# Kernel optimization log

Hardware: AMD Instinct MI355X
Metric: run time of the kernel (lower is better)

## Reference

```python
import jax, jax.numpy as jnp
import numpy as np

B, N, IN_DIM, HID, OUT, E = 2, 50000, 64, 256, 128, 500000

def setup_inputs() -> dict:
    key = jax.random.key(0)
    ks = jax.random.split(key, 8)
    s = lambda fan_in: 1.0 / np.sqrt(fan_in)
    x = jax.random.normal(ks[0], (B, N, IN_DIM), dtype=jnp.float32)
    edges = jax.random.randint(ks[1], (E, 2), 0, N, dtype=jnp.int64)
    return {
        "x": x,
        "edges": edges,
        "ew1": jax.random.normal(ks[2], (2 * IN_DIM, HID), dtype=jnp.float32) * s(2 * IN_DIM),
        "eb1": jnp.zeros((HID,), jnp.float32),
        "ew2": jax.random.normal(ks[3], (HID, OUT), dtype=jnp.float32) * s(HID),
        "eb2": jnp.zeros((OUT,), jnp.float32),
        "nw1": jax.random.normal(ks[4], (IN_DIM, HID), dtype=jnp.float32) * s(IN_DIM),
        "nb1": jnp.zeros((HID,), jnp.float32),
        "nw2": jax.random.normal(ks[5], (HID, OUT), dtype=jnp.float32) * s(HID),
        "nb2": jnp.zeros((OUT,), jnp.float32),
        "dw": jax.random.normal(ks[6], (OUT, IN_DIM), dtype=jnp.float32) * s(OUT),
        "db": jnp.zeros((IN_DIM,), jnp.float32),
    }

def _mlp(z, w1, b1, w2, b2):
    return jax.nn.relu(z @ w1 + b1) @ w2 + b2

def reference(x, edges, ew1, eb1, ew2, eb2, nw1, nb1, nw2, nb2, dw, db):
    u, v = edges[:, 0], edges[:, 1]
    # node embedding: [B, N, OUT]
    h = _mlp(x, nw1, nb1, nw2, nb2)
    # per-edge MLP on concatenated endpoint features: [B, E, OUT]
    edge_input = jnp.concatenate([x[:, u], x[:, v]], axis=-1)  # [B, E, 2*IN]
    edge_emb = _mlp(edge_input, ew1, eb1, ew2, eb2)
    # scatter-add edge message to both endpoints
    messages = jnp.zeros_like(h).at[:, u].add(edge_emb).at[:, v].add(edge_emb)
    h = h + messages
    recon = h @ dw + db  # [B, N, IN]
    return recon
```

## Files before the change

### kernel.cpp

```cpp
#include <hip/hip_runtime.h>
#include <hip/hip_bf16.h>

#define BB   2
#define NN   50000
#define BN   100000
#define NE   500000
#define NSB  196

using u16 = unsigned short;
using u32 = unsigned int;
typedef __attribute__((ext_vector_type(8))) short short8;
typedef __attribute__((ext_vector_type(8))) _Float16 half8;
typedef __attribute__((ext_vector_type(4))) float f32x4;

__device__ __forceinline__ u16 f2bf(float f) {
    union { float f; u32 u; } w; w.f = f;
    return (u16)((w.u + 0x7fffu + ((w.u >> 16) & 1u)) >> 16);
}
__device__ __forceinline__ u16 f2h(float f) {
    _Float16 h = (_Float16)f; u16 u; __builtin_memcpy(&u, &h, 2); return u;
}

#if defined(__has_builtin)
#if __has_builtin(__builtin_amdgcn_cvt_pk_bf16_f32)
#define HAVE_CVTPK 1
#endif
#if __has_builtin(__builtin_amdgcn_cvt_pkrtz)
#define HAVE_PKRTZ 1
#endif
#endif

__device__ __forceinline__ u32 pack_bf(float lo, float hi) {
#ifdef HAVE_CVTPK
    auto r = __builtin_amdgcn_cvt_pk_bf16_f32(lo, hi);
    u32 out; __builtin_memcpy(&out, &r, sizeof(out));
    return out;
#else
    return ((u32)f2bf(hi) << 16) | (u32)f2bf(lo);
#endif
}

__device__ __forceinline__ u32 pack_h2(float lo, float hi) {
#ifdef HAVE_PKRTZ
    auto r = __builtin_amdgcn_cvt_pkrtz(lo, hi);
    u32 out; __builtin_memcpy(&out, &r, sizeof(out));
    return out;
#else
    return ((u32)f2h(hi) << 16) | (u32)f2h(lo);
#endif
}

__device__ __forceinline__ u32 pk_add_h2(u32 a, u32 b) {
    u32 d; asm("v_pk_add_f16 %0, %1, %2" : "=v"(d) : "v"(a), "v"(b)); return d;
}
__device__ __forceinline__ u32 pk_relu_h2(u32 a) {
    u32 d, z = 0u;
    asm("v_pk_max_f16 %0, %1, %2" : "=v"(d) : "v"(a), "v"(z)); return d;
}
__device__ __forceinline__ half8 as_h8(short8 s) {
    half8 h; __builtin_memcpy(&h, &s, 16); return h;
}

__global__ __launch_bounds__(256) void csr_zero2(int* __restrict__ a, int* __restrict__ b) {
    int i = blockIdx.x * 256 + threadIdx.x;
    if (i < NN) { a[i] = 0; b[i] = 0; }
}

__global__ __launch_bounds__(256) void csr_hist2(const int* __restrict__ edges,
                                                 int* __restrict__ curU,
                                                 int* __restrict__ curV) {
    int e = blockIdx.x * 256 + threadIdx.x;
    if (e < NE) {
        atomicAdd(&curU[edges[2*e]], 1);
        atomicAdd(&curV[edges[2*e+1]], 1);
    }
}

__global__ __launch_bounds__(256) void scan_pass1(const int* __restrict__ cursor,
                                                  int* __restrict__ bsum) {
    __shared__ int s[256];
    const int t = threadIdx.x;
    int i = blockIdx.x * 256 + t;
    s[t] = (i < NN) ? cursor[i] : 0;
    __syncthreads();
    for (int d = 128; d > 0; d >>= 1) {
        if (t < d) s[t] += s[t + d];
        __syncthreads();
    }
    if (t == 0) bsum[blockIdx.x] = s[0];
}

__global__ __launch_bounds__(256) void scan_pass2(const int* __restrict__ bsum,
                                                  int* __restrict__ boff) {
    __shared__ int s[256];
    const int t = threadIdx.x;
    s[t] = (t < NSB) ? bsum[t] : 0;
    __syncthreads();
    for (int d = 1; d < 256; d <<= 1) {
        int v = (t >= d) ? s[t - d] : 0;
        __syncthreads();
        s[t] += v;
        __syncthreads();
    }
    if (t <= NSB) boff[t] = (t == 0) ? 0 : s[t - 1];
}

__global__ __launch_bounds__(256) void scan_pass3(int* __restrict__ cursor,
                                                  const int* __restrict__ boff,
                                                  int* __restrict__ off) {
    __shared__ int s[256];
    const int t = threadIdx.x;
    int i = blockIdx.x * 256 + t;
    int v = (i < NN) ? cursor[i] : 0;
    s[t] = v;
    __syncthreads();
    for (int d = 1; d < 256; d <<= 1) {
        int p = (t >= d) ? s[t - d] : 0;
        __syncthreads();
        s[t] += p;
        __syncthreads();
    }
    int excl = boff[blockIdx.x] + s[t] - v;
    if (i < NN) { off[i] = excl; cursor[i] = excl; }
    if (i == NN - 1) off[NN] = excl + v;
}

__global__ __launch_bounds__(256) void csr_fillU(const int* __restrict__ edges,
                                                 int* __restrict__ curU,
                                                 int* __restrict__ ueidx,
                                                 int* __restrict__ upos) {
    int e = blockIdx.x * 256 + threadIdx.x;
    if (e < NE) {
        int s = atomicAdd(&curU[edges[2*e]], 1);
        ueidx[s] = e;
        upos[e] = s;
    }
}

__global__ __launch_bounds__(256) void csr_fillV(const int* __restrict__ edges,
                                                 int* __restrict__ curV,
                                                 const int* __restrict__ upos,
                                                 int* __restrict__ vmap) {
    int e = blockIdx.x * 256 + threadIdx.x;
    if (e < NE) {
        int s = atomicAdd(&curV[edges[2*e+1]], 1);
        vmap[s] = upos[e];
    }
}

__global__ __launch_bounds__(256) void weight_prep(
    const float* __restrict__ ew1, const float* __restrict__ nw1,
    const float* __restrict__ ew2, const float* __restrict__ nw2,
    const float* __restrict__ dw,  const float* __restrict__ db,
    const float* __restrict__ eb2, const float* __restrict__ nb2,
    u16* __restrict__ frag, float* __restrict__ bias2)
{
    int blk = blockIdx.x, t = threadIdx.x;
    if (blk < 192) {
        int idx = blk * 256 + t;
        const float* src; int KB, local;
        if (idx < 32768) { local = idx;         src = ew1; KB = 4; }
        else             { local = idx - 32768; src = nw1; KB = 2; }
        int j = local & 7, l = (local >> 3) & 63, rest = local >> 9;
        int kblk = rest % KB, ntile = rest / KB;
        int n = ntile * 16 + (l & 15);
        int k = kblk * 32 + ((l >> 4) << 3) + j;
        frag[idx] = f2bf(src[k * 256 + n]);
    } else if (blk < 320) {
        int idx = (blk - 192) * 256 + t;
        bool is_e = (idx < 16384);
        const float* src = is_e ? ew2 : nw2;
        int local = idx & 16383;
        int j = local & 7, l = (local >> 3) & 63, rest = local >> 9;
        int kblk = rest & 7, ntile = rest >> 3;
        int n = ntile * 16 + (l & 15);
        int k = kblk * 32 + ((l >> 4) << 3) + j;
        float s = 0.f;
        for (int jj = 0; jj < 128; ++jj) s = fmaf(src[k * 128 + jj], dw[jj * 64 + n], s);
        frag[49152 + idx] = is_e ? f2h(s) : f2bf(s);
    } else if (t < 128) {
        int d = t & 63;
        const float* bsrc = (t >= 64) ? nb2 : eb2;
        float s = 0.f;
        #pragma unroll 4
        for (int j = 0; j < 128; ++j) s = fmaf(bsrc[j], dw[j * 64 + d], s);
        if (t >= 64) bias2[64 + d] = s + db[d];
        else         bias2[d] = s;
    }
}

__global__ __launch_bounds__(256) void node_mlp_kernel(
    const float* __restrict__ x, const float* __restrict__ nb1,
    const float* __restrict__ bias2, const u16* __restrict__ frag,
    u16* __restrict__ xbf, float* __restrict__ out)
{
    __shared__ u16 xs[64 * 64];
    __shared__ u16 hid[64 * 256];
    const int t = threadIdx.x;
    const int wave = t >> 6, l = t & 63, lane15 = l & 15, quad = l >> 4;
    const int r0 = blockIdx.x * 64;
    const int valid = min(64, BN - r0);

    #pragma unroll
    for (int it = 0; it < 4; ++it) {
        int i = t + it * 256;
        int m = i >> 4, c4 = i & 15;
        int row = min(r0 + m, BN - 1);
        float4 g = ((const float4*)x)[(size_t)row * 16 + c4];
        uint2 q = make_uint2(pack_bf(g.x, g.y), pack_bf(g.z, g.w));
        int chunk = c4 >> 1;
        *(uint2*)(xs + m * 64 + ((chunk ^ (m & 7)) << 3) + (c4 & 1) * 4) = q;
        *(uint2*)(xbf + (size_t)row * 64 + c4 * 4) = q;
    }
    __syncthreads();

    {
        f32x4 acc[4][4];
        #pragma unroll
        for (int i = 0; i < 4; ++i)
            #pragma unroll
            for (int mt = 0; mt < 4; ++mt) acc[i][mt] = f32x4{0.f,0.f,0.f,0.f};
        const u16* w1 = frag + 32768;
        #pragma unroll
        for (int kblk = 0; kblk < 2; ++kblk) {
            short8 bf[4], af[4];
            int chunk = kblk * 4 + quad;
            #pragma unroll
            for (int mt = 0; mt < 4; ++mt) {
                int row = mt*16 + lane15;
                bf[mt] = *(const short8*)(xs + row * 64 + ((chunk ^ (row & 7)) << 3));
            }
            #pragma unroll
            for (int i = 0; i < 4; ++i)
                af[i] = *(const short8*)(w1 + (((wave*4 + i)*2 + kblk)*64 + l) * 8);
            #pragma unroll
            for (int i = 0; i < 4; ++i)
                #pragma unroll
                for (int mt = 0; mt < 4; ++mt)
                    acc[i][mt] = __builtin_amdgcn_mfma_f32_16x16x32_bf16(af[i], bf[mt], acc[i][mt], 0, 0, 0);
        }
        #pragma unroll
        for (int i = 0; i < 4; ++i) {
            int n0 = (wave*4 + i)*16 + quad*4;
            int chunk = (wave*4 + i)*2 + (quad >> 1);
            float4 bv = *(const float4*)(nb1 + n0);
            #pragma unroll
            for (int mt = 0; mt < 4; ++mt) {
                int row = mt*16 + lane15;
                uint2 q = make_uint2(
                    pack_bf(fmaxf(acc[i][mt][0] + bv.x, 0.f), fmaxf(acc[i][mt][1] + bv.y, 0.f)),
                    pack_bf(fmaxf(acc[i][mt][2] + bv.z, 0.f), fmaxf(acc[i][mt][3] + bv.w, 0.f)));
                *(uint2*)(hid + row * 256 + ((chunk ^ (row & 15)) << 3) + (quad & 1) * 4) = q;
            }
        }
    }
    __syncthreads();

    {
        f32x4 acc[4];
        #pragma unroll
        for (int mt = 0; mt < 4; ++mt) acc[mt] = f32x4{0.f,0.f,0.f,0.f};
        const u16* w2 = frag + 65536;
        #pragma unroll
        for (int kblk = 0; kblk < 8; ++kblk) {
            short8 bf[4], af;
            int chunk = kblk * 4 + quad;
            #pragma unroll
            for (int mt = 0; mt < 4; ++mt) {
                int row = mt*16 + lane15;
                bf[mt] = *(const short8*)(hid + row * 256 + ((chunk ^ (row & 15)) << 3));
            }
            af = *(const short8*)(w2 + ((wave*8 + kblk)*64 + l) * 8);
            #pragma unroll
            for (int mt = 0; mt < 4; ++mt)
                acc[mt] = __builtin_amdgcn_mfma_f32_16x16x32_bf16(af, bf[mt], acc[mt], 0, 0, 0);
        }
        int n0 = wave*16 + quad*4;
        float4 bv = *(const float4*)(bias2 + 64 + n0);
        #pragma unroll
        for (int mt = 0; mt < 4; ++mt) {
            int m = mt*16 + lane15;
            if (m < valid) {
                float4 o;
                o.x = acc[mt][0] + bv.x; o.y = acc[mt][1] + bv.y;
                o.z = acc[mt][2] + bv.z; o.w = acc[mt][3] + bv.w;
                *(float4*)(out + (size_t)(r0 + m) * 64 + n0) = o;
            }
        }
    }
}

__global__ __launch_bounds__(256) void edge_pre_kernel(
    const u16* __restrict__ xbf, const float* __restrict__ eb1,
    const u16* __restrict__ frag, u16* __restrict__ At, u16* __restrict__ Ab,
    int b)
{
    __shared__ u16 xs[64 * 64];
    __shared__ u16 stg[64 * 256];
    const int t = threadIdx.x;
    const int wave = t >> 6, l = t & 63, lane15 = l & 15, quad = l >> 4;
    const int r0 = blockIdx.x * 64;
    const int valid = min(64, NN - r0);

    #pragma unroll
    for (int it = 0; it < 2; ++it) {
        int i = t + it * 256;
        int m = i >> 3, c = i & 7;
        int row = min(r0 + m, NN - 1);
        uint4 q = ((const uint4*)xbf)[((size_t)(b * NN + row)) * 8 + c];
        *(uint4*)(xs + m * 64 + ((c ^ (m & 7)) << 3)) = q;
    }
    __syncthreads();

    const u16* w1 = frag;
    for (int T = 0; T < 2; ++T) {
        f32x4 acc[4][4];
        #pragma unroll
        for (int i = 0; i < 4; ++i)
            #pragma unroll
            for (int mt = 0; mt < 4; ++mt) acc[i][mt] = f32x4{0.f,0.f,0.f,0.f};
        #pragma unroll
        for (int kblk = 0; kblk < 2; ++kblk) {
            short8 bf[4], af[4];
            int chunk = kblk * 4 + quad;
            #pragma unroll
            for (int mt = 0; mt < 4; ++mt) {
                int row = mt*16 + lane15;
                bf[mt] = *(const short8*)(xs + row * 64 + ((chunk ^ (row & 7)) << 3));
            }
            #pragma unroll
            for (int i = 0; i < 4; ++i)
                af[i] = *(const short8*)(w1 + (((wave*4 + i)*4 + T*2 + kblk)*64 + l) * 8);
            #pragma unroll
            for (int i = 0; i < 4; ++i)
                #pragma unroll
                for (int mt = 0; mt < 4; ++mt)
                    acc[i][mt] = __builtin_amdgcn_mfma_f32_16x16x32_bf16(af[i], bf[mt], acc[i][mt], 0, 0, 0);
        }
        #pragma unroll
        for (int i = 0; i < 4; ++i) {
            int ntile = wave*4 + i;
            int n0 = ntile*16 + quad*4;
            float4 bv;
            if (T == 0) bv = *(const float4*)(eb1 + n0);
            else        bv = make_float4(0.f, 0.f, 0.f, 0.f);
            int c16 = ntile*2 + (quad >> 1);
            #pragma unroll
            for (int mt = 0; mt < 4; ++mt) {
                int row = mt*16 + lane15;
                uint2 q = make_uint2(
                    pack_h2(acc[i][mt][0] + bv.x, acc[i][mt][1] + bv.y),
                    pack_h2(acc[i][mt][2] + bv.z, acc[i][mt][3] + bv.w));
                *(uint2*)(stg + row * 256 + ((c16 ^ (row & 7)) << 3) + (quad & 1) * 4) = q;
            }
        }
        __syncthreads();
        u16* dst = (T == 0) ? At : Ab;
        #pragma unroll
        for (int it = 0; it < 8; ++it) {
            int i = t + it * 256;
            int m = i >> 5, c = i & 31;
            if (m < valid)
                ((uint4*)dst)[((size_t)(r0 + m)) * 32 + c] =
                    *(const uint4*)(stg + m * 256 + ((c ^ (m & 7)) << 3));
        }
        __syncthreads();
    }
}

__global__ __launch_bounds__(256) void edge_emb2_kernel(
    const u16* __restrict__ At, const u16* __restrict__ Ab,
    const int* __restrict__ edges, const int* __restrict__ ueidx,
    const float* __restrict__ bias2,
    const u16* __restrict__ frag, u16* __restrict__ perm)
{
    __shared__ u16 hid[64 * 128];
    __shared__ int us[64], vs[64];
    const int t = threadIdx.x;
    const int wave = t >> 6, l = t & 63, lane15 = l & 15, quad = l >> 4;
    const int e0 = blockIdx.x * 64;
    const int valid = min(64, NE - e0);

    if (t < 64) {
        int j = min(e0 + t, NE - 1);
        int e = ueidx[j];
        us[t] = edges[2 * e];
        vs[t] = edges[2 * e + 1];
    }
    __syncthreads();

    f32x4 acc[4];
    #pragma unroll
    for (int mt = 0; mt < 4; ++mt) acc[mt] = f32x4{0.f,0.f,0.f,0.f};
    const u16* w2 = frag + 49152;

    #pragma unroll
    for (int half = 0; half < 2; ++half) {
        #pragma unroll
        for (int it = 0; it < 4; ++it) {
            int i = t + it * 256;
            int m = i >> 4, c = i & 15;
            int cg = half * 16 + c;
            int u = us[m], v = vs[m];
            uint4 a = ((const uint4*)At)[(size_t)((u32)u) * 32 + cg];
            uint4 bq = ((const uint4*)Ab)[(size_t)((u32)v) * 32 + cg];
            uint4 r;
            r.x = pk_relu_h2(pk_add_h2(a.x, bq.x));
            r.y = pk_relu_h2(pk_add_h2(a.y, bq.y));
            r.z = pk_relu_h2(pk_add_h2(a.z, bq.z));
            r.w = pk_relu_h2(pk_add_h2(a.w, bq.w));
            *(uint4*)(hid + m * 128 + ((c ^ (m & 15)) << 3)) = r;
        }
        __syncthreads();

        #pragma unroll
        for (int kb = 0; kb < 4; ++kb) {
            short8 bf[4], af;
            int chunk = kb * 4 + quad;
            #pragma unroll
            for (int mt = 0; mt < 4; ++mt) {
                int row = mt*16 + lane15;
                bf[mt] = *(const short8*)(hid + row * 128 + ((chunk ^ (row & 15)) << 3));
            }
            af = *(const short8*)(w2 + ((wave*8 + half*4 + kb)*64 + l) * 8);
            #pragma unroll
            for (int mt = 0; mt < 4; ++mt)
                acc[mt] = __builtin_amdgcn_mfma_f32_16x16x32_f16(as_h8(af), as_h8(bf[mt]), acc[mt], 0, 0, 0);
        }
        __syncthreads();
    }

    {
        int n0 = wave*16 + quad*4;
        int chunk = wave*2 + (quad >> 1);
        float4 bv = *(const float4*)(bias2 + n0);
        #pragma unroll
        for (int mt = 0; mt < 4; ++mt) {
            int m = mt*16 + lane15;
            uint2 q = make_uint2(
                pack_bf(acc[mt][0] + bv.x, acc[mt][1] + bv.y),
                pack_bf(acc[mt][2] + bv.z, acc[mt][3] + bv.w));
            *(uint2*)(hid + m * 64 + ((chunk ^ (m & 7)) << 3) + (quad & 1) * 4) = q;
        }
    }
    __syncthreads();

    #pragma unroll
    for (int it = 0; it < 2; ++it) {
        int i = t + it * 256;
        int m = i >> 3, c8 = i & 7;
        if (m < valid)
            ((uint4*)perm)[((size_t)(e0 + m)) * 8 + c8] =
                *(const uint4*)(hid + m * 64 + ((c8 ^ (m & 7)) << 3));
    }
}

__global__ __launch_bounds__(256) void gather3_kernel(
    const u32* __restrict__ perm32, const int* __restrict__ uoff,
    const int* __restrict__ voff, const int* __restrict__ vmap,
    float* __restrict__ out, int b)
{
    const int t = threadIdx.x, wave = t >> 6, l = t & 63;
    const int n = blockIdx.x * 4 + wave;
    const int ub = uoff[n], ucnt = uoff[n + 1] - ub;
    const int vb = voff[n], vcnt = voff[n + 1] - vb;
    if ((ucnt | vcnt) == 0) return;
    const int slot = l >> 4, c8h = l & 15;
    float a0 = 0.f, a1 = 0.f, a2 = 0.f, a3 = 0.f;

    for (int j0 = 0; j0 < ucnt; j0 += 8) {
        int jA = j0 + slot, jB = j0 + 4 + slot;
        const u32* rpA = perm32 + (size_t)(ub + min(jA, ucnt - 1)) * 32 + 2 * c8h;
        const u32* rpB = perm32 + (size_t)(ub + min(jB, ucnt - 1)) * 32 + 2 * c8h;
        u32 wA0 = rpA[0], wA1 = rpA[1];
        u32 wB0 = rpB[0], wB1 = rpB[1];
        union { u32 u; float f; } x0, x1, x2, x3;
        if (jA < ucnt) {
            x0.u = wA0 << 16; x1.u = wA0 & 0xffff0000u;
            x2.u = wA1 << 16; x3.u = wA1 & 0xffff0000u;
            a0 += x0.f; a1 += x1.f; a2 += x2.f; a3 += x3.f;
        }
        if (jB < ucnt) {
            x0.u = wB0 << 16; x1.u = wB0 & 0xffff0000u;
            x2.u = wB1 << 16; x3.u = wB1 & 0xffff0000u;
            a0 += x0.f; a1 += x1.f; a2 += x2.f; a3 += x3.f;
        }
    }
    for (int j0 = 0; j0 < vcnt; j0 += 8) {
        int jA = j0 + slot, jB = j0 + 4 + slot;
        int pA = vmap[vb + min(jA, vcnt - 1)];
        int pB = vmap[vb + min(jB, vcnt - 1)];
        const u32* rpA = perm32 + (size_t)pA * 32 + 2 * c8h;
        const u32* rpB = perm32 + (size_t)pB * 32 + 2 * c8h;
        u32 wA0 = rpA[0], wA1 = rpA[1];
        u32 wB0 = rpB[0], wB1 = rpB[1];
        union { u32 u; float f; } x0, x1, x2, x3;
        if (jA < vcnt) {
            x0.u = wA0 << 16; x1.u = wA0 & 0xffff0000u;
            x2.u = wA1 << 16; x3.u = wA1 & 0xffff0000u;
            a0 += x0.f; a1 += x1.f; a2 += x2.f; a3 += x3.f;
        }
        if (jB < vcnt) {
            x0.u = wB0 << 16; x1.u = wB0 & 0xffff0000u;
            x2.u = wB1 << 16; x3.u = wB1 & 0xffff0000u;
            a0 += x0.f; a1 += x1.f; a2 += x2.f; a3 += x3.f;
        }
    }

    a0 += __shfl_xor(a0, 16); a1 += __shfl_xor(a1, 16);
    a2 += __shfl_xor(a2, 16); a3 += __shfl_xor(a3, 16);
    a0 += __shfl_xor(a0, 32); a1 += __shfl_xor(a1, 32);
    a2 += __shfl_xor(a2, 32); a3 += __shfl_xor(a3, 32);
    if (l < 16) {
        float4* p = (float4*)(out + (size_t)(b * NN + n) * 64 + 4 * l);
        float4 h = *p;
        h.x += a0; h.y += a1; h.z += a2; h.w += a3;
        *p = h;
    }
}

extern "C" void kernel_launch(void* const* d_in, const int* in_sizes, int n_in,
                              void* d_out, int out_size, void* d_ws, size_t ws_size,
                              hipStream_t stream) {
    const float* x     = (const float*)d_in[0];
    const int*   edges = (const int*)d_in[1];
    const float* ew1   = (const float*)d_in[2];
    const float* eb1   = (const float*)d_in[3];
    const float* ew2   = (const float*)d_in[4];
    const float* eb2   = (const float*)d_in[5];
    const float* nw1   = (const float*)d_in[6];
    const float* nb1   = (const float*)d_in[7];
    const float* nw2   = (const float*)d_in[8];
    const float* nb2   = (const float*)d_in[9];
    const float* dw    = (const float*)d_in[10];
    const float* db    = (const float*)d_in[11];
    float* out = (float*)d_out;

    char* w = (char*)d_ws;
    size_t o = 0;
    auto take = [&](size_t bytes) { char* p = w + o; o = (o + bytes + 511) & ~(size_t)511; return p; };
    u16*   frag   = (u16*)  take(81920 * 2);
    float* bias2  = (float*)take(128 * 4);
    int*   curU   = (int*)  take((size_t)NN * 4);
    int*   curV   = (int*)  take((size_t)NN * 4);
    int*   uoff   = (int*)  take((size_t)(NN + 1) * 4);
    int*   voff   = (int*)  take((size_t)(NN + 1) * 4);
    int*   bsum   = (int*)  take((size_t)(NSB + 1) * 4);
    int*   boff   = (int*)  take((size_t)(NSB + 1) * 4);
    int*   ueidx  = (int*)  take((size_t)NE * 4);
    int*   upos   = (int*)  take((size_t)NE * 4);
    int*   vmap   = (int*)  take((size_t)NE * 4);
    u16*   xbf    = (u16*)  take((size_t)BN * 64 * 2);
    u16*   At     = (u16*)  take((size_t)NN * 256 * 2);
    u16*   Ab     = (u16*)  take((size_t)NN * 256 * 2);
    u16*   perm   = (u16*)  take((size_t)NE * 64 * 2);

    csr_zero2<<<NSB, 256, 0, stream>>>(curU, curV);
    csr_hist2<<<(NE + 255) / 256, 256, 0, stream>>>(edges, curU, curV);
    scan_pass1<<<NSB, 256, 0, stream>>>(curU, bsum);
    scan_pass2<<<1, 256, 0, stream>>>(bsum, boff);
    scan_pass3<<<NSB, 256, 0, stream>>>(curU, boff, uoff);
    scan_pass1<<<NSB, 256, 0, stream>>>(curV, bsum);
    scan_pass2<<<1, 256, 0, stream>>>(bsum, boff);
    scan_pass3<<<NSB, 256, 0, stream>>>(curV, boff, voff);
    csr_fillU<<<(NE + 255) / 256, 256, 0, stream>>>(edges, curU, ueidx, upos);
    csr_fillV<<<(NE + 255) / 256, 256, 0, stream>>>(edges, curV, upos, vmap);

    weight_prep<<<321, 256, 0, stream>>>(ew1, nw1, ew2, nw2, dw, db, eb2, nb2, frag, bias2);

    node_mlp_kernel<<<(BN + 63) / 64, 256, 0, stream>>>(x, nb1, bias2, frag, xbf, out);

    for (int b = 0; b < BB; ++b) {
        edge_pre_kernel<<<(NN + 63) / 64, 256, 0, stream>>>(xbf, eb1, frag, At, Ab, b);
        edge_emb2_kernel<<<(NE + 63) / 64, 256, 0, stream>>>(At, Ab, edges, ueidx, bias2, frag, perm);
        gather3_kernel<<<NN / 4, 256, 0, stream>>>((const u32*)perm, uoff, voff, vmap, out, b);
    }
}
```

Measured before the change: 457.5 us.

## Fuse CSR build, node MLP and edge precompute; process both batches per edge launch

Folds the edge-degree histogram into the weight-prep launch and the first scan pass into the node MLP launch. The node MLP kernel now also computes the per-node edge first-layer projections (At/Ab) for both batches, which removes the separate xbf buffer and the edge_pre kernel. The edge embedding and gather kernels handle both batches in one launch, storing u/v pairs in CSR order and gathering 128-wide rows. This cuts the number of launches and lets the per-edge and per-node index work be shared across batches, at the cost of larger intermediate buffers and more work per block.

New measurement: 407.3 us. 1.12x faster.

```diff
diff --git a/kernel.cpp b/kernel.cpp
--- a/kernel.cpp
+++ b/kernel.cpp
@@ -6,6 +6,7 @@
 #define BN   100000
 #define NE   500000
 #define NSB  196
+#define NODE_NB 1563
 
 using u16 = unsigned short;
 using u32 = unsigned int;
@@ -61,101 +62,23 @@
     half8 h; __builtin_memcpy(&h, &s, 16); return h;
 }
 
-__global__ __launch_bounds__(256) void csr_zero2(int* __restrict__ a, int* __restrict__ b) {
-    int i = blockIdx.x * 256 + threadIdx.x;
-    if (i < NN) { a[i] = 0; b[i] = 0; }
-}
-
-__global__ __launch_bounds__(256) void csr_hist2(const int* __restrict__ edges,
-                                                 int* __restrict__ curU,
-                                                 int* __restrict__ curV) {
-    int e = blockIdx.x * 256 + threadIdx.x;
-    if (e < NE) {
-        atomicAdd(&curU[edges[2*e]], 1);
-        atomicAdd(&curV[edges[2*e+1]], 1);
-    }
-}
-
-__global__ __launch_bounds__(256) void scan_pass1(const int* __restrict__ cursor,
-                                                  int* __restrict__ bsum) {
-    __shared__ int s[256];
-    const int t = threadIdx.x;
-    int i = blockIdx.x * 256 + t;
-    s[t] = (i < NN) ? cursor[i] : 0;
-    __syncthreads();
-    for (int d = 128; d > 0; d >>= 1) {
-        if (t < d) s[t] += s[t + d];
-        __syncthreads();
-    }
-    if (t == 0) bsum[blockIdx.x] = s[0];
-}
-
-__global__ __launch_bounds__(256) void scan_pass2(const int* __restrict__ bsum,
-                                                  int* __restrict__ boff) {
-    __shared__ int s[256];
-    const int t = threadIdx.x;
-    s[t] = (t < NSB) ? bsum[t] : 0;
-    __syncthreads();
-    for (int d = 1; d < 256; d <<= 1) {
-        int v = (t >= d) ? s[t - d] : 0;
-        __syncthreads();
-        s[t] += v;
-        __syncthreads();
-    }
-    if (t <= NSB) boff[t] = (t == 0) ? 0 : s[t - 1];
-}
-
-__global__ __launch_bounds__(256) void scan_pass3(int* __restrict__ cursor,
-                                                  const int* __restrict__ boff,
-                                                  int* __restrict__ off) {
-    __shared__ int s[256];
-    const int t = threadIdx.x;
-    int i = blockIdx.x * 256 + t;
-    int v = (i < NN) ? cursor[i] : 0;
-    s[t] = v;
-    __syncthreads();
-    for (int d = 1; d < 256; d <<= 1) {
-        int p = (t >= d) ? s[t - d] : 0;
-        __syncthreads();
-        s[t] += p;
-        __syncthreads();
-    }
-    int excl = boff[blockIdx.x] + s[t] - v;
-    if (i < NN) { off[i] = excl; cursor[i] = excl; }
-    if (i == NN - 1) off[NN] = excl + v;
-}
-
-__global__ __launch_bounds__(256) void csr_fillU(const int* __restrict__ edges,
-                                                 int* __restrict__ curU,
-                                                 int* __restrict__ ueidx,
-                                                 int* __restrict__ upos) {
-    int e = blockIdx.x * 256 + threadIdx.x;
-    if (e < NE) {
-        int s = atomicAdd(&curU[edges[2*e]], 1);
-        ueidx[s] = e;
-        upos[e] = s;
-    }
-}
-
-__global__ __launch_bounds__(256) void csr_fillV(const int* __restrict__ edges,
-                                                 int* __restrict__ curV,
-                                                 const int* __restrict__ upos,
-                                                 int* __restrict__ vmap) {
-    int e = blockIdx.x * 256 + threadIdx.x;
-    if (e < NE) {
-        int s = atomicAdd(&curV[edges[2*e+1]], 1);
-        vmap[s] = upos[e];
-    }
-}
-
-__global__ __launch_bounds__(256) void weight_prep(
+__global__ __launch_bounds__(256) void weight_prep_hist(
     const float* __restrict__ ew1, const float* __restrict__ nw1,
     const float* __restrict__ ew2, const float* __restrict__ nw2,
     const float* __restrict__ dw,  const float* __restrict__ db,
     const float* __restrict__ eb2, const float* __restrict__ nb2,
+    const int* __restrict__ edges, int* __restrict__ curU, int* __restrict__ curV,
     u16* __restrict__ frag, float* __restrict__ bias2)
 {
     int blk = blockIdx.x, t = threadIdx.x;
+    if (blk >= 321) {
+        int e = (blk - 321) * 256 + t;
+        if (e < NE) {
+            atomicAdd(&curU[edges[2*e]], 1);
+            atomicAdd(&curV[edges[2*e+1]], 1);
+        }
+        return;
+    }
     if (blk < 192) {
         int idx = blk * 256 + t;
         const float* src; int KB, local;
@@ -189,14 +112,90 @@
     }
 }
 
+__global__ __launch_bounds__(256) void scan_pass2d(const int* __restrict__ bsum2,
+                                                   int* __restrict__ boff2) {
+    __shared__ int s[256];
+    const int t = threadIdx.x;
+    const int base = blockIdx.y * (NSB + 1);
+    s[t] = (t < NSB) ? bsum2[base + t] : 0;
+    __syncthreads();
+    for (int d = 1; d < 256; d <<= 1) {
+        int v = (t >= d) ? s[t - d] : 0;
+        __syncthreads();
+        s[t] += v;
+        __syncthreads();
+    }
+    if (t <= NSB) boff2[base + t] = (t == 0) ? 0 : s[t - 1];
+}
+
+__global__ __launch_bounds__(256) void scan_pass3d(int* __restrict__ curU,
+                                                   int* __restrict__ curV,
+                                                   const int* __restrict__ boff2,
+                                                   int* __restrict__ uoff,
+                                                   int* __restrict__ voff) {
+    __shared__ int s[256];
+    const int t = threadIdx.x;
+    int* cursor = blockIdx.y ? curV : curU;
+    int* off    = blockIdx.y ? voff : uoff;
+    const int base = blockIdx.y * (NSB + 1);
+    int i = blockIdx.x * 256 + t;
+    int v = (i < NN) ? cursor[i] : 0;
+    s[t] = v;
+    __syncthreads();
+    for (int d = 1; d < 256; d <<= 1) {
+        int p = (t >= d) ? s[t - d] : 0;
+        __syncthreads();
+        s[t] += p;
+        __syncthreads();
+    }
+    int excl = boff2[base + blockIdx.x] + s[t] - v;
+    if (i < NN) { off[i] = excl; cursor[i] = excl; }
+    if (i == NN - 1) off[NN] = excl + v;
+}
+
+__global__ __launch_bounds__(256) void csr_fill2(const int* __restrict__ edges,
+                                                 int* __restrict__ curU,
+                                                 int* __restrict__ curV,
+                                                 int2* __restrict__ uv,
+                                                 int* __restrict__ vmap) {
+    int e = blockIdx.x * 256 + threadIdx.x;
+    if (e < NE) {
+        int u = edges[2*e], v = edges[2*e+1];
+        int s0 = atomicAdd(&curU[u], 1);
+        uv[s0] = make_int2(u, v);
+        int s1 = atomicAdd(&curV[v], 1);
+        vmap[s1] = s0;
+    }
+}
+
 __global__ __launch_bounds__(256) void node_mlp_kernel(
     const float* __restrict__ x, const float* __restrict__ nb1,
-    const float* __restrict__ bias2, const u16* __restrict__ frag,
-    u16* __restrict__ xbf, float* __restrict__ out)
+    const float* __restrict__ eb1, const float* __restrict__ bias2,
+    const u16* __restrict__ frag,
+    u16* __restrict__ At, u16* __restrict__ Ab, float* __restrict__ out,
+    const int* __restrict__ curU, const int* __restrict__ curV,
+    int* __restrict__ bsum2)
 {
     __shared__ u16 xs[64 * 64];
-    __shared__ u16 hid[64 * 256];
+    __shared__ u16 hid[64 * 128];
     const int t = threadIdx.x;
+
+    if (blockIdx.x >= NODE_NB) {
+        int sb = blockIdx.x - NODE_NB;
+        int y = sb / NSB, xi = sb - y * NSB;
+        const int* cursor = y ? curV : curU;
+        int* s = (int*)xs;
+        int i = xi * 256 + t;
+        s[t] = (i < NN) ? cursor[i] : 0;
+        __syncthreads();
+        for (int d = 128; d > 0; d >>= 1) {
+            if (t < d) s[t] += s[t + d];
+            __syncthreads();
+        }
+        if (t == 0) bsum2[y * (NSB + 1) + xi] = s[0];
+        return;
+    }
+
     const int wave = t >> 6, l = t & 63, lane15 = l & 15, quad = l >> 4;
     const int r0 = blockIdx.x * 64;
     const int valid = min(64, BN - r0);
@@ -210,20 +209,24 @@
         uint2 q = make_uint2(pack_bf(g.x, g.y), pack_bf(g.z, g.w));
         int chunk = c4 >> 1;
         *(uint2*)(xs + m * 64 + ((chunk ^ (m & 7)) << 3) + (c4 & 1) * 4) = q;
-        *(uint2*)(xbf + (size_t)row * 64 + c4 * 4) = q;
     }
     __syncthreads();
 
-    {
-        f32x4 acc[4][4];
-        #pragma unroll
-        for (int i = 0; i < 4; ++i)
-            #pragma unroll
-            for (int mt = 0; mt < 4; ++mt) acc[i][mt] = f32x4{0.f,0.f,0.f,0.f};
-        const u16* w1 = frag + 32768;
+    f32x4 acc2[4];
+    #pragma unroll
+    for (int mt = 0; mt < 4; ++mt) acc2[mt] = f32x4{0.f,0.f,0.f,0.f};
+    const u16* w1n = frag + 32768;
+    const u16* w2n = frag + 65536;
+    #pragma unroll
+    for (int H = 0; H < 2; ++H) {
+        f32x4 acc1[2][4];
+        #pragma unroll
+        for (int i = 0; i < 2; ++i)
+            #pragma unroll
+            for (int mt = 0; mt < 4; ++mt) acc1[i][mt] = f32x4{0.f,0.f,0.f,0.f};
         #pragma unroll
         for (int kblk = 0; kblk < 2; ++kblk) {
-            short8 bf[4], af[4];
+            short8 bf[4], af[2];
             int chunk = kblk * 4 + quad;
             #pragma unroll
             for (int mt = 0; mt < 4; ++mt) {
@@ -231,50 +234,47 @@
                 bf[mt] = *(const short8*)(xs + row * 64 + ((chunk ^ (row & 7)) << 3));
             }
             #pragma unroll
-            for (int i = 0; i < 4; ++i)
-                af[i] = *(const short8*)(w1 + (((wave*4 + i)*2 + kblk)*64 + l) * 8);
-            #pragma unroll
-            for (int i = 0; i < 4; ++i)
+            for (int i = 0; i < 2; ++i)
+                af[i] = *(const short8*)(w1n + (((H*8 + wave*2 + i)*2 + kblk)*64 + l) * 8);
+            #pragma unroll
+            for (int i = 0; i < 2; ++i)
                 #pragma unroll
                 for (int mt = 0; mt < 4; ++mt)
-                    acc[i][mt] = __builtin_amdgcn_mfma_f32_16x16x32_bf16(af[i], bf[mt], acc[i][mt], 0, 0, 0);
-        }
-        #pragma unroll
-        for (int i = 0; i < 4; ++i) {
-            int n0 = (wave*4 + i)*16 + quad*4;
-            int chunk = (wave*4 + i)*2 + (quad >> 1);
+                    acc1[i][mt] = __builtin_amdgcn_mfma_f32_16x16x32_bf16(af[i], bf[mt], acc1[i][mt], 0, 0, 0);
+        }
+        #pragma unroll
+        for (int i = 0; i < 2; ++i) {
+            int ntl = wave*2 + i;
+            int n0 = (H*8 + ntl)*16 + quad*4;
+            int c16 = ntl*2 + (quad >> 1);
             float4 bv = *(const float4*)(nb1 + n0);
             #pragma unroll
             for (int mt = 0; mt < 4; ++mt) {
                 int row = mt*16 + lane15;
                 uint2 q = make_uint2(
-                    pack_bf(fmaxf(acc[i][mt][0] + bv.x, 0.f), fmaxf(acc[i][mt][1] + bv.y, 0.f)),
-                    pack_bf(fmaxf(acc[i][mt][2] + bv.z, 0.f), fmaxf(acc[i][mt][3] + bv.w, 0.f)));
-                *(uint2*)(hid + row * 256 + ((chunk ^ (row & 15)) << 3) + (quad & 1) * 4) = q;
-            }
-        }
-    }
-    __syncthreads();
-
-    {
-        f32x4 acc[4];
-        #pragma unroll
-        for (int mt = 0; mt < 4; ++mt) acc[mt] = f32x4{0.f,0.f,0.f,0.f};
-        const u16* w2 = frag + 65536;
-        #pragma unroll
-        for (int kblk = 0; kblk < 8; ++kblk) {
+                    pack_bf(fmaxf(acc1[i][mt][0] + bv.x, 0.f), fmaxf(acc1[i][mt][1] + bv.y, 0.f)),
+                    pack_bf(fmaxf(acc1[i][mt][2] + bv.z, 0.f), fmaxf(acc1[i][mt][3] + bv.w, 0.f)));
+                *(uint2*)(hid + row * 128 + ((c16 ^ (row & 15)) << 3) + (quad & 1) * 4) = q;
+            }
+        }
+        __syncthreads();
+        #pragma unroll
+        for (int kb = 0; kb < 4; ++kb) {
             short8 bf[4], af;
-            int chunk = kblk * 4 + quad;
+            int chunk = kb * 4 + quad;
             #pragma unroll
             for (int mt = 0; mt < 4; ++mt) {
                 int row = mt*16 + lane15;
-                bf[mt] = *(const short8*)(hid + row * 256 + ((chunk ^ (row & 15)) << 3));
-            }
-            af = *(const short8*)(w2 + ((wave*8 + kblk)*64 + l) * 8);
+                bf[mt] = *(const short8*)(hid + row * 128 + ((chunk ^ (row & 15)) << 3));
+            }
+            af = *(const short8*)(w2n + ((wave*8 + H*4 + kb)*64 + l) * 8);
             #pragma unroll
             for (int mt = 0; mt < 4; ++mt)
-                acc[mt] = __builtin_amdgcn_mfma_f32_16x16x32_bf16(af, bf[mt], acc[mt], 0, 0, 0);
-        }
+                acc2[mt] = __builtin_amdgcn_mfma_f32_16x16x32_bf16(af, bf[mt], acc2[mt], 0, 0, 0);
+        }
+        __syncthreads();
+    }
+    {
         int n0 = wave*16 + quad*4;
         float4 bv = *(const float4*)(bias2 + 64 + n0);
         #pragma unroll
@@ -282,96 +282,76 @@
             int m = mt*16 + lane15;
             if (m < valid) {
                 float4 o;
-                o.x = acc[mt][0] + bv.x; o.y = acc[mt][1] + bv.y;
-                o.z = acc[mt][2] + bv.z; o.w = acc[mt][3] + bv.w;
+                o.x = acc2[mt][0] + bv.x; o.y = acc2[mt][1] + bv.y;
+                o.z = acc2[mt][2] + bv.z; o.w = acc2[mt][3] + bv.w;
                 *(float4*)(out + (size_t)(r0 + m) * 64 + n0) = o;
             }
         }
     }
-}
-
-__global__ __launch_bounds__(256) void edge_pre_kernel(
-    const u16* __restrict__ xbf, const float* __restrict__ eb1,
-    const u16* __restrict__ frag, u16* __restrict__ At, u16* __restrict__ Ab,
-    int b)
-{
-    __shared__ u16 xs[64 * 64];
-    __shared__ u16 stg[64 * 256];
-    const int t = threadIdx.x;
-    const int wave = t >> 6, l = t & 63, lane15 = l & 15, quad = l >> 4;
-    const int r0 = blockIdx.x * 64;
-    const int valid = min(64, NN - r0);
-
-    #pragma unroll
-    for (int it = 0; it < 2; ++it) {
-        int i = t + it * 256;
-        int m = i >> 3, c = i & 7;
-        int row = min(r0 + m, NN - 1);
-        uint4 q = ((const uint4*)xbf)[((size_t)(b * NN + row)) * 8 + c];
-        *(uint4*)(xs + m * 64 + ((c ^ (m & 7)) << 3)) = q;
-    }
-    __syncthreads();
-
-    const u16* w1 = frag;
+
+    const u16* w1e = frag;
+    #pragma unroll
     for (int T = 0; T < 2; ++T) {
-        f32x4 acc[4][4];
-        #pragma unroll
-        for (int i = 0; i < 4; ++i)
-            #pragma unroll
-            for (int mt = 0; mt < 4; ++mt) acc[i][mt] = f32x4{0.f,0.f,0.f,0.f};
-        #pragma unroll
-        for (int kblk = 0; kblk < 2; ++kblk) {
-            short8 bf[4], af[4];
-            int chunk = kblk * 4 + quad;
-            #pragma unroll
-            for (int mt = 0; mt < 4; ++mt) {
-                int row = mt*16 + lane15;
-                bf[mt] = *(const short8*)(xs + row * 64 + ((chunk ^ (row & 7)) << 3));
-            }
-            #pragma unroll
-            for (int i = 0; i < 4; ++i)
-                af[i] = *(const short8*)(w1 + (((wave*4 + i)*4 + T*2 + kblk)*64 + l) * 8);
-            #pragma unroll
-            for (int i = 0; i < 4; ++i)
-                #pragma unroll
-                for (int mt = 0; mt < 4; ++mt)
-                    acc[i][mt] = __builtin_amdgcn_mfma_f32_16x16x32_bf16(af[i], bf[mt], acc[i][mt], 0, 0, 0);
-        }
-        #pragma unroll
-        for (int i = 0; i < 4; ++i) {
-            int ntile = wave*4 + i;
-            int n0 = ntile*16 + quad*4;
-            float4 bv;
-            if (T == 0) bv = *(const float4*)(eb1 + n0);
-            else        bv = make_float4(0.f, 0.f, 0.f, 0.f);
-            int c16 = ntile*2 + (quad >> 1);
-            #pragma unroll
-            for (int mt = 0; mt < 4; ++mt) {
-                int row = mt*16 + lane15;
-                uint2 q = make_uint2(
-                    pack_h2(acc[i][mt][0] + bv.x, acc[i][mt][1] + bv.y),
-                    pack_h2(acc[i][mt][2] + bv.z, acc[i][mt][3] + bv.w));
-                *(uint2*)(stg + row * 256 + ((c16 ^ (row & 7)) << 3) + (quad & 1) * 4) = q;
-            }
-        }
-        __syncthreads();
-        u16* dst = (T == 0) ? At : Ab;
-        #pragma unroll
-        for (int it = 0; it < 8; ++it) {
-            int i = t + it * 256;
-            int m = i >> 5, c = i & 31;
-            if (m < valid)
-                ((uint4*)dst)[((size_t)(r0 + m)) * 32 + c] =
-                    *(const uint4*)(stg + m * 256 + ((c ^ (m & 7)) << 3));
-        }
-        __syncthreads();
-    }
-}
-
-__global__ __launch_bounds__(256) void edge_emb2_kernel(
+        u16* dst = T ? Ab : At;
+        #pragma unroll
+        for (int H = 0; H < 2; ++H) {
+            f32x4 acc[2][4];
+            #pragma unroll
+            for (int i = 0; i < 2; ++i)
+                #pragma unroll
+                for (int mt = 0; mt < 4; ++mt) acc[i][mt] = f32x4{0.f,0.f,0.f,0.f};
+            #pragma unroll
+            for (int kblk = 0; kblk < 2; ++kblk) {
+                short8 bf[4], af[2];
+                int chunk = kblk * 4 + quad;
+                #pragma unroll
+                for (int mt = 0; mt < 4; ++mt) {
+                    int row = mt*16 + lane15;
+                    bf[mt] = *(const short8*)(xs + row * 64 + ((chunk ^ (row & 7)) << 3));
+                }
+                #pragma unroll
+                for (int i = 0; i < 2; ++i)
+                    af[i] = *(const short8*)(w1e + (((H*8 + wave*2 + i)*4 + T*2 + kblk)*64 + l) * 8);
+                #pragma unroll
+                for (int i = 0; i < 2; ++i)
+                    #pragma unroll
+                    for (int mt = 0; mt < 4; ++mt)
+                        acc[i][mt] = __builtin_amdgcn_mfma_f32_16x16x32_bf16(af[i], bf[mt], acc[i][mt], 0, 0, 0);
+            }
+            #pragma unroll
+            for (int i = 0; i < 2; ++i) {
+                int ntl = wave*2 + i;
+                int n0 = (H*8 + ntl)*16 + quad*4;
+                int c16 = ntl*2 + (quad >> 1);
+                float4 bv;
+                if (T == 0) bv = *(const float4*)(eb1 + n0);
+                else        bv = make_float4(0.f, 0.f, 0.f, 0.f);
+                #pragma unroll
+                for (int mt = 0; mt < 4; ++mt) {
+                    int row = mt*16 + lane15;
+                    uint2 q = make_uint2(
+                        pack_h2(acc[i][mt][0] + bv.x, acc[i][mt][1] + bv.y),
+                        pack_h2(acc[i][mt][2] + bv.z, acc[i][mt][3] + bv.w));
+                    *(uint2*)(hid + row * 128 + ((c16 ^ (row & 15)) << 3) + (quad & 1) * 4) = q;
+                }
+            }
+            __syncthreads();
+            #pragma unroll
+            for (int it = 0; it < 4; ++it) {
+                int i = t + it * 256;
+                int m = i >> 4, c = i & 15;
+                if (m < valid)
+                    ((uint4*)dst)[((size_t)(r0 + m)) * 32 + H*16 + c] =
+                        *(const uint4*)(hid + m * 128 + ((c ^ (m & 15)) << 3));
+            }
+            __syncthreads();
+        }
+    }
+}
+
+__global__ __launch_bounds__(256) void edge_emb3_kernel(
     const u16* __restrict__ At, const u16* __restrict__ Ab,
-    const int* __restrict__ edges, const int* __restrict__ ueidx,
-    const float* __restrict__ bias2,
+    const int2* __restrict__ uv, const float* __restrict__ bias2,
     const u16* __restrict__ frag, u16* __restrict__ perm)
 {
     __shared__ u16 hid[64 * 128];
@@ -382,140 +362,142 @@
     const int valid = min(64, NE - e0);
 
     if (t < 64) {
-        int j = min(e0 + t, NE - 1);
-        int e = ueidx[j];
-        us[t] = edges[2 * e];
-        vs[t] = edges[2 * e + 1];
+        int2 p = uv[min(e0 + t, NE - 1)];
+        us[t] = p.x;
+        vs[t] = p.y;
     }
     __syncthreads();
 
-    f32x4 acc[4];
-    #pragma unroll
-    for (int mt = 0; mt < 4; ++mt) acc[mt] = f32x4{0.f,0.f,0.f,0.f};
     const u16* w2 = frag + 49152;
-
-    #pragma unroll
-    for (int half = 0; half < 2; ++half) {
-        #pragma unroll
-        for (int it = 0; it < 4; ++it) {
-            int i = t + it * 256;
-            int m = i >> 4, c = i & 15;
-            int cg = half * 16 + c;
-            int u = us[m], v = vs[m];
-            uint4 a = ((const uint4*)At)[(size_t)((u32)u) * 32 + cg];
-            uint4 bq = ((const uint4*)Ab)[(size_t)((u32)v) * 32 + cg];
-            uint4 r;
-            r.x = pk_relu_h2(pk_add_h2(a.x, bq.x));
-            r.y = pk_relu_h2(pk_add_h2(a.y, bq.y));
-            r.z = pk_relu_h2(pk_add_h2(a.z, bq.z));
-            r.w = pk_relu_h2(pk_add_h2(a.w, bq.w));
-            *(uint4*)(hid + m * 128 + ((c ^ (m & 15)) << 3)) = r;
-        }
-        __syncthreads();
-
-        #pragma unroll
-        for (int kb = 0; kb < 4; ++kb) {
-            short8 bf[4], af;
-            int chunk = kb * 4 + quad;
-            #pragma unroll
-            for (int mt = 0; mt < 4; ++mt) {
-                int row = mt*16 + lane15;
-                bf[mt] = *(const short8*)(hid + row * 128 + ((chunk ^ (row & 15)) << 3));
-            }
-            af = *(const short8*)(w2 + ((wave*8 + half*4 + kb)*64 + l) * 8);
-            #pragma unroll
-            for (int mt = 0; mt < 4; ++mt)
-                acc[mt] = __builtin_amdgcn_mfma_f32_16x16x32_f16(as_h8(af), as_h8(bf[mt]), acc[mt], 0, 0, 0);
-        }
-        __syncthreads();
+    f32x4 accB[2][4];
+    #pragma unroll
+    for (int b = 0; b < 2; ++b)
+        #pragma unroll
+        for (int mt = 0; mt < 4; ++mt) accB[b][mt] = f32x4{0.f,0.f,0.f,0.f};
+
+    #pragma unroll
+    for (int b = 0; b < 2; ++b) {
+        const u16* Atb = At + (size_t)b * NN * 256;
+        const u16* Abb = Ab + (size_t)b * NN * 256;
+        #pragma unroll
+        for (int half = 0; half < 2; ++half) {
+            #pragma unroll
+            for (int it = 0; it < 4; ++it) {
+                int i = t + it * 256;
+                int m = i >> 4, c = i & 15;
+                int cg = half * 16 + c;
+                int u = us[m], v = vs[m];
+                uint4 a = ((const uint4*)Atb)[(size_t)((u32)u) * 32 + cg];
+                uint4 bq = ((const uint4*)Abb)[(size_t)((u32)v) * 32 + cg];
+                uint4 r;
+                r.x = pk_relu_h2(pk_add_h2(a.x, bq.x));
+                r.y = pk_relu_h2(pk_add_h2(a.y, bq.y));
+                r.z = pk_relu_h2(pk_add_h2(a.z, bq.z));
+                r.w = pk_relu_h2(pk_add_h2(a.w, bq.w));
+                *(uint4*)(hid + m * 128 + ((c ^ (m & 15)) << 3)) = r;
+            }
+            __syncthreads();
+            #pragma unroll
+            for (int kb = 0; kb < 4; ++kb) {
+                short8 bf[4], af;
+                int chunk = kb * 4 + quad;
+                #pragma unroll
+                for (int mt = 0; mt < 4; ++mt) {
+                    int row = mt*16 + lane15;
+                    bf[mt] = *(const short8*)(hid + row * 128 + ((chunk ^ (row & 15)) << 3));
+                }
+                af = *(const short8*)(w2 + ((wave*8 + half*4 + kb)*64 + l) * 8);
+                #pragma unroll
+                for (int mt = 0; mt < 4; ++mt)
+                    accB[b][mt] = __builtin_amdgcn_mfma_f32_16x16x32_f16(as_h8(af), as_h8(bf[mt]), accB[b][mt], 0, 0, 0);
+            }
+            __syncthreads();
+        }
     }
 
     {
         int n0 = wave*16 + quad*4;
-        int chunk = wave*2 + (quad >> 1);
         float4 bv = *(const float4*)(bias2 + n0);
         #pragma unroll
-        for (int mt = 0; mt < 4; ++mt) {
-            int m = mt*16 + lane15;
-            uint2 q = make_uint2(
-                pack_bf(acc[mt][0] + bv.x, acc[mt][1] + bv.y),
-                pack_bf(acc[mt][2] + bv.z, acc[mt][3] + bv.w));
-            *(uint2*)(hid + m * 64 + ((chunk ^ (m & 7)) << 3) + (quad & 1) * 4) = q;
+        for (int b = 0; b < 2; ++b) {
+            int cc = b*8 + wave*2 + (quad >> 1);
+            #pragma unroll
+            for (int mt = 0; mt < 4; ++mt) {
+                int m = mt*16 + lane15;
+                uint2 q = make_uint2(
+                    pack_bf(accB[b][mt][0] + bv.x, accB[b][mt][1] + bv.y),
+                    pack_bf(accB[b][mt][2] + bv.z, accB[b][mt][3] + bv.w));
+                *(uint2*)(hid + m * 128 + ((cc ^ (m & 15)) << 3) + (quad & 1) * 4) = q;
+            }
         }
     }
     __syncthreads();
 
     #pragma unroll
-    for (int it = 0; it < 2; ++it) {
+    for (int it = 0; it < 4; ++it) {
         int i = t + it * 256;
-        int m = i >> 3, c8 = i & 7;
+        int m = i >> 4, c = i & 15;
         if (m < valid)
-            ((uint4*)perm)[((size_t)(e0 + m)) * 8 + c8] =
-                *(const uint4*)(hid + m * 64 + ((c8 ^ (m & 7)) << 3));
-    }
-}
-
-__global__ __launch_bounds__(256) void gather3_kernel(
+            ((uint4*)perm)[((size_t)(e0 + m)) * 16 + c] =
+                *(const uint4*)(hid + m * 128 + ((c ^ (m & 15)) << 3));
+    }
+}
+
+#define ACCUM8(q) { union { u32 u; float f; } xx;                         \
+    xx.u = (q).x << 16;          a0 += xx.f;                              \
+    xx.u = (q).x & 0xffff0000u;  a1 += xx.f;                              \
+    xx.u = (q).y << 16;          a2 += xx.f;                              \
+    xx.u = (q).y & 0xffff0000u;  a3 += xx.f;                              \
+    xx.u = (q).z << 16;          a4 += xx.f;                              \
+    xx.u = (q).z & 0xffff0000u;  a5 += xx.f;                              \
+    xx.u = (q).w << 16;          a6 += xx.f;                              \
+    xx.u = (q).w & 0xffff0000u;  a7 += xx.f; }
+
+__global__ __launch_bounds__(256) void gather4_kernel(
     const u32* __restrict__ perm32, const int* __restrict__ uoff,
     const int* __restrict__ voff, const int* __restrict__ vmap,
-    float* __restrict__ out, int b)
+    float* __restrict__ out)
 {
     const int t = threadIdx.x, wave = t >> 6, l = t & 63;
     const int n = blockIdx.x * 4 + wave;
     const int ub = uoff[n], ucnt = uoff[n + 1] - ub;
     const int vb = voff[n], vcnt = voff[n + 1] - vb;
     if ((ucnt | vcnt) == 0) return;
-    const int slot = l >> 4, c8h = l & 15;
-    float a0 = 0.f, a1 = 0.f, a2 = 0.f, a3 = 0.f;
+    const int sg = l >> 4, c16 = l & 15;
+    float a0=0.f,a1=0.f,a2=0.f,a3=0.f,a4=0.f,a5=0.f,a6=0.f,a7=0.f;
 
     for (int j0 = 0; j0 < ucnt; j0 += 8) {
-        int jA = j0 + slot, jB = j0 + 4 + slot;
-        const u32* rpA = perm32 + (size_t)(ub + min(jA, ucnt - 1)) * 32 + 2 * c8h;
-        const u32* rpB = perm32 + (size_t)(ub + min(jB, ucnt - 1)) * 32 + 2 * c8h;
-        u32 wA0 = rpA[0], wA1 = rpA[1];
-        u32 wB0 = rpB[0], wB1 = rpB[1];
-        union { u32 u; float f; } x0, x1, x2, x3;
-        if (jA < ucnt) {
-            x0.u = wA0 << 16; x1.u = wA0 & 0xffff0000u;
-            x2.u = wA1 << 16; x3.u = wA1 & 0xffff0000u;
-            a0 += x0.f; a1 += x1.f; a2 += x2.f; a3 += x3.f;
-        }
-        if (jB < ucnt) {
-            x0.u = wB0 << 16; x1.u = wB0 & 0xffff0000u;
-            x2.u = wB1 << 16; x3.u = wB1 & 0xffff0000u;
-            a0 += x0.f; a1 += x1.f; a2 += x2.f; a3 += x3.f;
-        }
+        int jA = j0 + sg, jB = j0 + 4 + sg;
+        uint4 qA = *(const uint4*)(perm32 + (size_t)(ub + min(jA, ucnt - 1)) * 64 + c16 * 4);
+        uint4 qB = *(const uint4*)(perm32 + (size_t)(ub + min(jB, ucnt - 1)) * 64 + c16 * 4);
+        if (jA < ucnt) ACCUM8(qA);
+        if (jB < ucnt) ACCUM8(qB);
     }
     for (int j0 = 0; j0 < vcnt; j0 += 8) {
-        int jA = j0 + slot, jB = j0 + 4 + slot;
+        int jA = j0 + sg, jB = j0 + 4 + sg;
         int pA = vmap[vb + min(jA, vcnt - 1)];
         int pB = vmap[vb + min(jB, vcnt - 1)];
-        const u32* rpA = perm32 + (size_t)pA * 32 + 2 * c8h;
-        const u32* rpB = perm32 + (size_t)pB * 32 + 2 * c8h;
-        u32 wA0 = rpA[0], wA1 = rpA[1];
-        u32 wB0 = rpB[0], wB1 = rpB[1];
-        union { u32 u; float f; } x0, x1, x2, x3;
-        if (jA < vcnt) {
-            x0.u = wA0 << 16; x1.u = wA0 & 0xffff0000u;
-            x2.u = wA1 << 16; x3.u = wA1 & 0xffff0000u;
-            a0 += x0.f; a1 += x1.f; a2 += x2.f; a3 += x3.f;
-        }
-        if (jB < vcnt) {
-            x0.u = wB0 << 16; x1.u = wB0 & 0xffff0000u;
-            x2.u = wB1 << 16; x3.u = wB1 & 0xffff0000u;
-            a0 += x0.f; a1 += x1.f; a2 += x2.f; a3 += x3.f;
-        }
+        uint4 qA = *(const uint4*)(perm32 + (size_t)pA * 64 + c16 * 4);
+        uint4 qB = *(const uint4*)(perm32 + (size_t)pB * 64 + c16 * 4);
+        if (jA < vcnt) ACCUM8(qA);
+        if (jB < vcnt) ACCUM8(qB);
     }
 
     a0 += __shfl_xor(a0, 16); a1 += __shfl_xor(a1, 16);
     a2 += __shfl_xor(a2, 16); a3 += __shfl_xor(a3, 16);
+    a4 += __shfl_xor(a4, 16); a5 += __shfl_xor(a5, 16);
+    a6 += __shfl_xor(a6, 16); a7 += __shfl_xor(a7, 16);
     a0 += __shfl_xor(a0, 32); a1 += __shfl_xor(a1, 32);
     a2 += __shfl_xor(a2, 32); a3 += __shfl_xor(a3, 32);
+    a4 += __shfl_xor(a4, 32); a5 += __shfl_xor(a5, 32);
+    a6 += __shfl_xor(a6, 32); a7 += __shfl_xor(a7, 32);
+
     if (l < 16) {
-        float4* p = (float4*)(out + (size_t)(b * NN + n) * 64 + 4 * l);
-        float4 h = *p;
-        h.x += a0; h.y += a1; h.z += a2; h.w += a3;
-        *p = h;
+        float* p = out + ((size_t)((l >> 3) * NN + n)) * 64 + (l & 7) * 8;
+        float4 h0 = *(float4*)p, h1 = *(float4*)(p + 4);
+        h0.x += a0; h0.y += a1; h0.z += a2; h0.w += a3;
+        h1.x += a4; h1.y += a5; h1.z += a6; h1.w += a7;
+        *(float4*)p = h0; *(float4*)(p + 4) = h1;
     }
 }
 
@@ -545,34 +527,29 @@
     int*   curV   = (int*)  take((size_t)NN * 4);
     int*   uoff   = (int*)  take((size_t)(NN + 1) * 4);
     int*   voff   = (int*)  take((size_t)(NN + 1) * 4);
-    int*   bsum   = (int*)  take((size_t)(NSB + 1) * 4);
-    int*   boff   = (int*)  take((size_t)(NSB + 1) * 4);
-    int*   ueidx  = (int*)  take((size_t)NE * 4);
-    int*   upos   = (int*)  take((size_t)NE * 4);
+    int*   bsum2  = (int*)  take((size_t)2 * (NSB + 1) * 4);
+    int*   boff2  = (int*)  take((size_t)2 * (NSB + 1) * 4);
     int*   vmap   = (int*)  take((size_t)NE * 4);
-    u16*   xbf    = (u16*)  take((size_t)BN * 64 * 2);
-    u16*   At     = (u16*)  take((size_t)NN * 256 * 2);
-    u16*   Ab     = (u16*)  take((size_t)NN * 256 * 2);
-    u16*   perm   = (u16*)  take((size_t)NE * 64 * 2);
-
-    csr_zero2<<<NSB, 256, 0, stream>>>(curU, curV);
-    csr_hist2<<<(NE + 255) / 256, 256, 0, stream>>>(edges, curU, curV);
-    scan_pass1<<<NSB, 256, 0, stream>>>(curU, bsum);
-    scan_pass2<<<1, 256, 0, stream>>>(bsum, boff);
-    scan_pass3<<<NSB, 256, 0, stream>>>(curU, boff, uoff);
-    scan_pass1<<<NSB, 256, 0, stream>>>(curV, bsum);
-    scan_pass2<<<1, 256, 0, stream>>>(bsum, boff);
-    scan_pass3<<<NSB, 256, 0, stream>>>(curV, boff, voff);
-    csr_fillU<<<(NE + 255) / 256, 256, 0, stream>>>(edges, curU, ueidx, upos);
-    csr_fillV<<<(NE + 255) / 256, 256, 0, stream>>>(edges, curV, upos, vmap);
-
-    weight_prep<<<321, 256, 0, stream>>>(ew1, nw1, ew2, nw2, dw, db, eb2, nb2, frag, bias2);
-
-    node_mlp_kernel<<<(BN + 63) / 64, 256, 0, stream>>>(x, nb1, bias2, frag, xbf, out);
-
-    for (int b = 0; b < BB; ++b) {
-        edge_pre_kernel<<<(NN + 63) / 64, 256, 0, stream>>>(xbf, eb1, frag, At, Ab, b);
-        edge_emb2_kernel<<<(NE + 63) / 64, 256, 0, stream>>>(At, Ab, edges, ueidx, bias2, frag, perm);
-        gather3_kernel<<<NN / 4, 256, 0, stream>>>((const u32*)perm, uoff, voff, vmap, out, b);
-    }
-}
+    int2*  uv     = (int2*) take((size_t)NE * 8);
+    u16*   At     = (u16*)  take((size_t)BN * 256 * 2);
+    u16*   Ab     = (u16*)  take((size_t)BN * 256 * 2);
+    u16*   perm   = (u16*)  take((size_t)NE * 128 * 2);
+    (void)ws_size;
+
+    hipMemsetAsync(curU, 0, (size_t)NN * 4, stream);
+    hipMemsetAsync(curV, 0, (size_t)NN * 4, stream);
+
+    weight_prep_hist<<<321 + (NE + 255) / 256, 256, 0, stream>>>(
+        ew1, nw1, ew2, nw2, dw, db, eb2, nb2, edges, curU, curV, frag, bias2);
+
+    node_mlp_kernel<<<NODE_NB + 2 * NSB, 256, 0, stream>>>(
+        x, nb1, eb1, bias2, frag, At, Ab, out, curU, curV, bsum2);
+
+    scan_pass2d<<<dim3(1, 2), 256, 0, stream>>>(bsum2, boff2);
+    scan_pass3d<<<dim3(NSB, 2), 256, 0, stream>>>(curU, curV, boff2, uoff, voff);
+    csr_fill2<<<(NE + 255) / 256, 256, 0, stream>>>(edges, curU, curV, uv, vmap);
+
+    edge_emb3_kernel<<<(NE + 63) / 64, 256, 0, stream>>>(At, Ab, uv, bias2, frag, perm);
+
+    gather4_kernel<<<NN / 4, 256, 0, stream>>>((const u32*)perm, uoff, voff, vmap, out);
+}
```
